# Performance work log

Measured on AMD Instinct MI355X. Metric: run time of the kernel, lower is better.

The kernel has to match this reference:

```python
import jax, jax.numpy as jnp
import numpy as np

N, E = 30000, 180000
IN, H, OUT = 3000, 512, 30


def _segment_softmax(e, dst, n):
    # numerically stable softmax over incoming edges of each destination node
    m = jax.ops.segment_max(e, dst, num_segments=n)
    m = jnp.where(jnp.isfinite(m), m, 0.0)  # nodes with no in-edges
    ex = jnp.exp(e - m[dst])
    den = jax.ops.segment_sum(ex, dst, num_segments=n)
    return ex / den[dst]


def _gat(x, src, dst, Ws, Wd, a_s, a_d, n, alpha=None):
    """edGATConv (heads=1, no self-loops, no bias).
    xs = lin_s(x); attention score from lin_s(x)[src] and lin_d(x)[dst];
    out[i] = sum_{e: dst_e=i} alpha_e * xs[src_e].
    If alpha is given (tie_alpha), reuse it instead of recomputing."""
    xs = x @ Ws.T  # [n, F_out]
    if alpha is None:
        xd = x @ Wd.T
        e = jax.nn.leaky_relu(xs[src] @ a_s + xd[dst] @ a_d, 0.2)  # [E]
        alpha = _segment_softmax(e, dst, n)
    out = jax.ops.segment_sum(alpha[:, None] * xs[src], dst, num_segments=n)
    return out, alpha


def setup_inputs() -> dict:
    key = jax.random.key(0)
    ks = jax.random.split(key, 7)
    features = jax.random.normal(ks[0], (N, IN), dtype=jnp.float32)
    edge_index = jax.random.randint(ks[1], (2, E), 0, N)
    W1s = jax.random.normal(ks[2], (H, IN), dtype=jnp.float32) * 0.02
    W1d = jax.random.normal(ks[3], (H, IN), dtype=jnp.float32) * 0.02
    a1s = jax.random.normal(ks[4], (H,), dtype=jnp.float32) * 0.1
    a1d = jax.random.normal(ks[5], (H,), dtype=jnp.float32) * 0.1
    W2s = jax.random.normal(ks[6], (OUT, H), dtype=jnp.float32) * 0.05
    return {"features": features, "edge_index": edge_index,
            "W1s": W1s, "W1d": W1d, "a1s": a1s, "a1d": a1d, "W2s": W2s}


def reference(features, edge_index, W1s, W1d, a1s, a1d, W2s):
    src, dst = edge_index[0], edge_index[1]
    n = features.shape[0]
    # conv1: attentive GAT layer, stores tie_alpha
    h1, alpha1 = _gat(features, src, dst, W1s, W1d, a1s, a1d, n)
    h1 = jax.nn.elu(h1)
    # conv2: aslinear=True -> plain linear with lin_s
    h2 = h1 @ W2s.T  # [N, OUT]
    # conv3: weights tied to conv2 transposed, alpha tied to conv1
    # W3s = W2s.T so xs3 = h2 @ W3s.T = h2 @ W2s
    h3, _ = _gat(h2, src, dst, W2s.T, None, None, None, n, alpha=alpha1)
    h3 = jax.nn.elu(h3)
    # conv4: aslinear, weight tied to conv1 transposed: h3 @ W4s.T = h3 @ W1s
    h4 = h3 @ W1s  # [N, IN]
    return (h2, h4)
```

## Files before the change

kernel.cpp:

```cpp
#include <hip/hip_runtime.h>

typedef unsigned short u16;
typedef __bf16 bf16_t;
typedef bf16_t bf16x8 __attribute__((ext_vector_type(8)));
typedef float f32x4 __attribute__((ext_vector_type(4)));
typedef u16 u16x8 __attribute__((ext_vector_type(8)));

#define AS1 __attribute__((address_space(1)))
#define AS3 __attribute__((address_space(3)))

__device__ __forceinline__ u16 f2bf(float f) {
    union { float f; unsigned u; } v; v.f = f;
    unsigned r = v.u + 0x7FFFu + ((v.u >> 16) & 1u);
    return (u16)(r >> 16);
}
__device__ __forceinline__ float bf2f(u16 s) {
    union { unsigned u; float f; } v; v.u = ((unsigned)s) << 16;
    return v.f;
}

__device__ __forceinline__ void gload_lds16(const u16* g, u16* l) {
    __builtin_amdgcn_global_load_lds((AS1 const void*)g, (AS3 void*)l, 16, 0, 0);
}

template <bool OUT_BF16, bool GUARD>
__global__ __launch_bounds__(256) void gemm_bt(
    const u16* __restrict__ A, const u16* __restrict__ B, void* __restrict__ Cv,
    int K, int ldc, int Mreal, int Nreal)
{
    __shared__ u16 As[128 * 64];
    __shared__ u16 Bs[128 * 64];
    const int t = threadIdx.x;
    const int w = t >> 6, l = t & 63;

    const int nwg = gridDim.x * gridDim.y;
    const int lin = blockIdx.y * gridDim.x + blockIdx.x;
    const int xcd = lin & 7, loc = lin >> 3;
    const int q = nwg >> 3, r = nwg & 7;
    const int swz = (xcd < r ? xcd * (q + 1) : r * (q + 1) + (xcd - r) * q) + loc;
    const int bx = swz % gridDim.x, by = swz / gridDim.x;

    const int m0 = by * 128, n0 = bx * 128;
    const int wm = (w >> 1) * 64, wn = (w & 1) * 64;

    const int srow = w << 5;
    const int lrow = l >> 3, lc = l & 7;

    f32x4 acc[4][4] = {};

    for (int kt = 0; kt < K; kt += 64) {
#pragma unroll
        for (int i = 0; i < 4; ++i) {
            int row = srow + i * 8 + lrow;
            int gc = ((lc ^ (row & 7)) << 3);
            const u16* ga = A + (size_t)(m0 + row) * K + kt + gc;
            const u16* gb = B + (size_t)(n0 + row) * K + kt + gc;
            u16* la = &As[(srow + i * 8) * 64];
            u16* lb = &Bs[(srow + i * 8) * 64];
            gload_lds16(ga, la);
            gload_lds16(gb, lb);
        }
        asm volatile("s_waitcnt vmcnt(0)");
        __syncthreads();

#pragma unroll
        for (int kk = 0; kk < 2; ++kk) {
            bf16x8 af[4], bfr[4];
            int kc = kk * 4 + (l >> 4);
#pragma unroll
            for (int mi = 0; mi < 4; ++mi) {
                int row = wm + mi * 16 + (l & 15);
                af[mi] = *(const bf16x8*)&As[row * 64 + ((kc ^ (row & 7)) << 3)];
            }
#pragma unroll
            for (int ni = 0; ni < 4; ++ni) {
                int col = wn + ni * 16 + (l & 15);
                bfr[ni] = *(const bf16x8*)&Bs[col * 64 + ((kc ^ (col & 7)) << 3)];
            }
#pragma unroll
            for (int mi = 0; mi < 4; ++mi)
#pragma unroll
                for (int ni = 0; ni < 4; ++ni)
                    acc[mi][ni] = __builtin_amdgcn_mfma_f32_16x16x32_bf16(
                        af[mi], bfr[ni], acc[mi][ni], 0, 0, 0);
        }
        __syncthreads();
    }

#pragma unroll
    for (int mi = 0; mi < 4; ++mi) {
#pragma unroll
        for (int qq = 0; qq < 4; ++qq) {
            int row = m0 + wm + mi * 16 + (l >> 4) * 4 + qq;
            if (GUARD && row >= Mreal) continue;
#pragma unroll
            for (int ni = 0; ni < 4; ++ni) {
                int col = n0 + wn + ni * 16 + (l & 15);
                if (GUARD && col >= Nreal) continue;
                float v = acc[mi][ni][qq];
                if (OUT_BF16) ((u16*)Cv)[(size_t)row * ldc + col] = f2bf(v);
                else          ((float*)Cv)[(size_t)row * ldc + col] = v;
            }
        }
    }
}

__global__ __launch_bounds__(256) void gemm_xw2(
    const float* __restrict__ X, const u16* __restrict__ Bw, u16* __restrict__ C,
    const float* __restrict__ vd, const float* __restrict__ vs,
    float* __restrict__ sd, float* __restrict__ ss)
{
    __shared__ u16 As[128 * 64];
    __shared__ u16 Bs[2][128 * 64];
    const int t = threadIdx.x;
    const int w = t >> 6, l = t & 63;

    const int nwg = gridDim.x * gridDim.y;
    const int lin = blockIdx.y * gridDim.x + blockIdx.x;
    const int xcd = lin & 7, loc = lin >> 3;
    const int q = nwg >> 3, r = nwg & 7;
    const int swz = (xcd < r ? xcd * (q + 1) : r * (q + 1) + (xcd - r) * q) + loc;
    const int bx = swz % gridDim.x, by = swz / gridDim.x;

    const int m0 = by * 128, n0 = bx * 128;
    const int wm = (w >> 1) * 64, wn = (w & 1) * 64;
    const int srow = w << 5;
    const int lrow = l >> 3, lc = l & 7;

    f32x4 acc[4][4] = {};
    float sdp[4] = {}, ssp[4] = {};
    const bool do_s = (bx == 0);

    int rowg[4];
    bool okr[4];
#pragma unroll
    for (int i = 0; i < 4; ++i) {
        rowg[i] = m0 + srow + i * 8 + lrow;
        okr[i] = rowg[i] < 30000;
    }

    float4 pa[4][2];
    auto loadA = [&](int kt) {
        int c = kt + lc * 8;
        bool okc = c < 3000;
#pragma unroll
        for (int i = 0; i < 4; ++i) {
            bool ok = okr[i] && okc;
            const float* p = X + (ok ? ((size_t)rowg[i] * 3000 + c) : 0);
            float4 v0 = *(const float4*)p;
            float4 v1 = *(const float4*)(p + 4);
            if (!ok) { v0 = make_float4(0.f, 0.f, 0.f, 0.f); v1 = v0; }
            pa[i][0] = v0;
            pa[i][1] = v1;
        }
    };
    auto stageB = [&](int kt2, int buf) {
#pragma unroll
        for (int i = 0; i < 4; ++i) {
            int row = srow + i * 8 + lrow;
            int gc = ((lc ^ (row & 7)) << 3);
            gload_lds16(Bw + (size_t)(n0 + row) * 3008 + kt2 + gc,
                        &Bs[buf][(srow + i * 8) * 64]);
        }
    };

    loadA(0);
    stageB(0, 0);
    int cur = 0;

    for (int kt = 0; kt < 3008; kt += 64) {
        if (do_s) {
            int c = kt + lc * 8;
            float4 d0 = *(const float4*)(vd + c);
            float4 d1 = *(const float4*)(vd + c + 4);
            float4 s0 = *(const float4*)(vs + c);
            float4 s1 = *(const float4*)(vs + c + 4);
#pragma unroll
            for (int i = 0; i < 4; ++i) {
                sdp[i] += pa[i][0].x * d0.x + pa[i][0].y * d0.y + pa[i][0].z * d0.z + pa[i][0].w * d0.w
                        + pa[i][1].x * d1.x + pa[i][1].y * d1.y + pa[i][1].z * d1.z + pa[i][1].w * d1.w;
                ssp[i] += pa[i][0].x * s0.x + pa[i][0].y * s0.y + pa[i][0].z * s0.z + pa[i][0].w * s0.w
                        + pa[i][1].x * s1.x + pa[i][1].y * s1.y + pa[i][1].z * s1.z + pa[i][1].w * s1.w;
            }
        }
#pragma unroll
        for (int i = 0; i < 4; ++i) {
            int row = srow + i * 8 + lrow;
            u16x8 o;
            o[0] = f2bf(pa[i][0].x); o[1] = f2bf(pa[i][0].y);
            o[2] = f2bf(pa[i][0].z); o[3] = f2bf(pa[i][0].w);
            o[4] = f2bf(pa[i][1].x); o[5] = f2bf(pa[i][1].y);
            o[6] = f2bf(pa[i][1].z); o[7] = f2bf(pa[i][1].w);
            *(u16x8*)&As[row * 64 + ((lc ^ (row & 7)) << 3)] = o;
        }
        loadA(kt + 64);
        int ktn = (kt + 64 < 3008) ? kt + 64 : 2944;
        stageB(ktn, cur ^ 1);
        asm volatile("s_waitcnt vmcnt(12) lgkmcnt(0)" ::: "memory");
        __builtin_amdgcn_s_barrier();

#pragma unroll
        for (int kk = 0; kk < 2; ++kk) {
            bf16x8 af[4], bfr[4];
            int kc = kk * 4 + (l >> 4);
#pragma unroll
            for (int mi = 0; mi < 4; ++mi) {
                int row = wm + mi * 16 + (l & 15);
                af[mi] = *(const bf16x8*)&As[row * 64 + ((kc ^ (row & 7)) << 3)];
            }
#pragma unroll
            for (int ni = 0; ni < 4; ++ni) {
                int col = wn + ni * 16 + (l & 15);
                bfr[ni] = *(const bf16x8*)&Bs[cur][col * 64 + ((kc ^ (col & 7)) << 3)];
            }
#pragma unroll
            for (int mi = 0; mi < 4; ++mi)
#pragma unroll
                for (int ni = 0; ni < 4; ++ni)
                    acc[mi][ni] = __builtin_amdgcn_mfma_f32_16x16x32_bf16(
                        af[mi], bfr[ni], acc[mi][ni], 0, 0, 0);
        }
        asm volatile("s_barrier" ::: "memory");
        cur ^= 1;
    }

    if (do_s) {
#pragma unroll
        for (int i = 0; i < 4; ++i) {
            float a = sdp[i], b = ssp[i];
            a += __shfl_xor(a, 1); a += __shfl_xor(a, 2); a += __shfl_xor(a, 4);
            b += __shfl_xor(b, 1); b += __shfl_xor(b, 2); b += __shfl_xor(b, 4);
            if (lc == 0 && okr[i]) { sd[rowg[i]] = a; ss[rowg[i]] = b; }
        }
    }

#pragma unroll
    for (int mi = 0; mi < 4; ++mi)
#pragma unroll
        for (int qq = 0; qq < 4; ++qq) {
            int row = m0 + wm + mi * 16 + (l >> 4) * 4 + qq;
#pragma unroll
            for (int ni = 0; ni < 4; ++ni) {
                int col = n0 + wn + ni * 16 + (l & 15);
                C[(size_t)row * 512 + col] = f2bf(acc[mi][qq == 0 ? ni : ni][qq]);
            }
        }
}

__global__ void k_prep(const float* __restrict__ W1d, const float* __restrict__ a1d,
                       const float* __restrict__ W1s, const float* __restrict__ a1s,
                       const float* __restrict__ W2s, const int* __restrict__ dst,
                       float* __restrict__ vd, float* __restrict__ vs,
                       u16* __restrict__ w1sb, u16* __restrict__ w1st,
                       u16* __restrict__ w2sb, unsigned* __restrict__ deg) {
    int b = blockIdx.x, t = threadIdx.x;
    if (b < 12) {
        int i = b * 256 + t;
        if (i >= 3000) return;
        float ad = 0.f, as = 0.f;
        for (int h = 0; h < 512; ++h) {
            ad += W1d[(size_t)h * 3000 + i] * a1d[h];
            as += W1s[(size_t)h * 3000 + i] * a1s[h];
        }
        vd[i] = ad;
        vs[i] = as;
    } else if (b < 1516) {
        int idx = (b - 12) * 256 + t;
        int n = idx / 752, k = (idx % 752) * 4;
        ushort4 o = make_ushort4(0, 0, 0, 0);
        if (k < 3000) {
            float4 v = *(const float4*)(W1s + (size_t)n * 3000 + k);
            o.x = f2bf(v.x); o.y = f2bf(v.y); o.z = f2bf(v.z); o.w = f2bf(v.w);
        }
        *(ushort4*)(w1sb + (size_t)n * 3008 + k) = o;
    } else if (b < 1900) {
        __shared__ float tile[64][65];
        int fb = b - 1516;
        int i0 = (fb % 48) * 64, h0 = (fb / 48) * 64;
        int il = t & 63, hq = t >> 6;
#pragma unroll
        for (int rr = 0; rr < 16; ++rr) {
            int hl = rr * 4 + hq;
            int i = i0 + il;
            tile[hl][il] = (i < 3000) ? W1s[(size_t)(h0 + hl) * 3000 + i] : 0.f;
        }
        __syncthreads();
#pragma unroll
        for (int rr = 0; rr < 16; ++rr) {
            int il2 = rr * 4 + hq;
            w1st[(size_t)(i0 + il2) * 512 + h0 + il] = f2bf(tile[il][il2]);
        }
    } else if (b < 2156) {
        int idx = (b - 1900) * 256 + t;
        int n = idx >> 9, k = idx & 511;
        w2sb[idx] = (n < 30) ? f2bf(W2s[(size_t)n * 512 + k]) : (u16)0;
    } else {
        int j = (b - 2156) * 256 + t;
        if (j < 180000) atomicAdd(&deg[dst[j]], 1u);
    }
}

__global__ void k_scan1(const unsigned* __restrict__ deg, unsigned* __restrict__ bsum, int n) {
    __shared__ unsigned ws[4];
    int i = blockIdx.x * 256 + threadIdx.x;
    unsigned v = (i < n) ? deg[i] : 0u;
#pragma unroll
    for (int s = 32; s; s >>= 1) v += __shfl_xor(v, s);
    if ((threadIdx.x & 63) == 0) ws[threadIdx.x >> 6] = v;
    __syncthreads();
    if (threadIdx.x == 0) bsum[blockIdx.x] = ws[0] + ws[1] + ws[2] + ws[3];
}

__global__ void k_scanB(const unsigned* __restrict__ deg, const unsigned* __restrict__ bsum,
                        unsigned* __restrict__ off, unsigned* __restrict__ cur,
                        int n, int nb) {
    __shared__ unsigned tmp[256];
    __shared__ unsigned bo;
    int b = blockIdx.x, t = threadIdx.x, i = b * 256 + t;
    if (t < 64) {
        unsigned s0 = (t < nb) ? bsum[t] : 0u;
        unsigned s1 = (t + 64 < nb) ? bsum[t + 64] : 0u;
        unsigned v = ((t < b) ? s0 : 0u) + ((t + 64 < b) ? s1 : 0u);
#pragma unroll
        for (int s = 32; s; s >>= 1) v += __shfl_xor(v, s);
        if (t == 0) bo = v;
        if (b == nb - 1) {
            unsigned tv = s0 + s1;
#pragma unroll
            for (int s = 32; s; s >>= 1) tv += __shfl_xor(tv, s);
            if (t == 0) off[n] = tv;
        }
    }
    __syncthreads();
    unsigned v = (i < n) ? deg[i] : 0u;
    tmp[t] = v;
    __syncthreads();
    for (int s = 1; s < 256; s <<= 1) {
        unsigned a = (t >= s) ? tmp[t - s] : 0u;
        __syncthreads();
        tmp[t] += a;
        __syncthreads();
    }
    if (i < n) {
        unsigned o = bo + tmp[t] - v;
        off[i] = o;
        cur[i] = o;
    }
}

__global__ void k_fill(const int* __restrict__ dst, unsigned* __restrict__ cur,
                       unsigned* __restrict__ csr) {
    int j = blockIdx.x * 256 + threadIdx.x;
    if (j >= 180000) return;
    unsigned pos = atomicAdd(&cur[dst[j]], 1u);
    csr[pos] = (unsigned)j;
}

__global__ void k_soft(const int* __restrict__ src, const float* __restrict__ ss,
                       const float* __restrict__ sd, float* __restrict__ alpha,
                       const unsigned* __restrict__ csr, const unsigned* __restrict__ off) {
    int t = threadIdx.x;
    int g = t >> 3, l = t & 7;
    int n = blockIdx.x * 32 + g;
    if (n >= 30000) return;
    unsigned lo = off[n], hi = off[n + 1];
    if (lo == hi) return;
    float sdn = sd[n];
    float m = -1e30f;
    for (unsigned i = lo + l; i < hi; i += 8) {
        float v = ss[src[csr[i]]] + sdn;
        v = v > 0.f ? v : 0.2f * v;
        m = fmaxf(m, v);
    }
    m = fmaxf(m, __shfl_xor(m, 1));
    m = fmaxf(m, __shfl_xor(m, 2));
    m = fmaxf(m, __shfl_xor(m, 4));
    float den = 0.f;
    for (unsigned i = lo + l; i < hi; i += 8) {
        float v = ss[src[csr[i]]] + sdn;
        v = v > 0.f ? v : 0.2f * v;
        den += expf(v - m);
    }
    den += __shfl_xor(den, 1);
    den += __shfl_xor(den, 2);
    den += __shfl_xor(den, 4);
    float inv = 1.f / den;
    for (unsigned i = lo + l; i < hi; i += 8) {
        unsigned j = csr[i];
        float v = ss[src[j]] + sdn;
        v = v > 0.f ? v : 0.2f * v;
        alpha[j] = expf(v - m) * inv;
    }
}

__global__ void k_agg(const u16* __restrict__ xin, const float* __restrict__ alpha,
                      const unsigned* __restrict__ csr, const unsigned* __restrict__ off,
                      const int* __restrict__ src, u16* __restrict__ outb, int nvalid) {
    int w = threadIdx.x >> 6, l = threadIdx.x & 63;
    int n = blockIdx.x * 4 + w;
    float acc[8] = {};
    if (n < nvalid) {
        unsigned lo = off[n], hi = off[n + 1];
        unsigned i = lo;
        for (; i + 2 <= hi; i += 2) {
            unsigned j0 = csr[i], j1 = csr[i + 1];
            float a0 = alpha[j0], a1 = alpha[j1];
            int s0 = src[j0], s1 = src[j1];
            u16x8 r0 = *(const u16x8*)&xin[(size_t)s0 * 512 + l * 8];
            u16x8 r1 = *(const u16x8*)&xin[(size_t)s1 * 512 + l * 8];
#pragma unroll
            for (int k = 0; k < 8; ++k) acc[k] += a0 * bf2f(r0[k]) + a1 * bf2f(r1[k]);
        }
        if (i < hi) {
            unsigned j0 = csr[i];
            float a0 = alpha[j0];
            int s0 = src[j0];
            u16x8 r0 = *(const u16x8*)&xin[(size_t)s0 * 512 + l * 8];
#pragma unroll
            for (int k = 0; k < 8; ++k) acc[k] += a0 * bf2f(r0[k]);
        }
    }
    u16x8 o;
#pragma unroll
    for (int k = 0; k < 8; ++k) {
        float a = acc[k] > 0.f ? acc[k] : expf(acc[k]) - 1.f;
        o[k] = f2bf(a);
    }
    *(u16x8*)&outb[(size_t)n * 512 + l * 8] = o;
}

__global__ void k_aggG(const float* __restrict__ h2, const float* __restrict__ alpha,
                       const unsigned* __restrict__ csr, const unsigned* __restrict__ off,
                       const int* __restrict__ src, float* __restrict__ g) {
    int t = threadIdx.x, grp = t >> 3, l = t & 7;
    int n = blockIdx.x * 32 + grp;
    if (n >= 30000) return;
    unsigned lo = off[n], hi = off[n + 1];
    float acc[4] = {};
    int c0 = l * 4;
    for (unsigned i = lo; i < hi; ++i) {
        unsigned j = csr[i];
        float a = alpha[j];
        const float* row = h2 + (size_t)src[j] * 30;
#pragma unroll
        for (int k = 0; k < 4; ++k) {
            int c = c0 + k;
            if (c < 30) acc[k] += a * row[c];
        }
    }
#pragma unroll
    for (int k = 0; k < 4; ++k) {
        int c = c0 + k;
        if (c < 30) g[(size_t)n * 30 + c] = acc[k];
    }
}

__global__ void k_h3(const float* __restrict__ g, const float* __restrict__ W2s,
                     u16* __restrict__ h3b) {
    int t = threadIdx.x;
    size_t n0 = (size_t)blockIdx.x * 8;
    float w0[30], w1[30];
#pragma unroll
    for (int o = 0; o < 30; ++o) {
        w0[o] = W2s[(size_t)o * 512 + t];
        w1[o] = W2s[(size_t)o * 512 + t + 256];
    }
    for (int rr = 0; rr < 8; ++rr) {
        size_t n = n0 + rr;
        float a0 = 0.f, a1 = 0.f;
        if (n < 30000) {
            const float* gr = g + n * 30;
#pragma unroll
            for (int o = 0; o < 30; ++o) {
                float v = gr[o];
                a0 += v * w0[o];
                a1 += v * w1[o];
            }
            a0 = a0 > 0.f ? a0 : expf(a0) - 1.f;
            a1 = a1 > 0.f ? a1 : expf(a1) - 1.f;
        }
        h3b[n * 512 + t] = f2bf(a0);
        h3b[n * 512 + t + 256] = f2bf(a1);
    }
}

extern "C" void kernel_launch(void* const* d_in, const int* in_sizes, int n_in,
                              void* d_out, int out_size, void* d_ws, size_t ws_size,
                              hipStream_t stream) {
    const float* X   = (const float*)d_in[0];
    const int*   ei  = (const int*)d_in[1];
    const float* W1s = (const float*)d_in[2];
    const float* W1d = (const float*)d_in[3];
    const float* a1s = (const float*)d_in[4];
    const float* a1d = (const float*)d_in[5];
    const float* W2s = (const float*)d_in[6];
    const int* src = ei;
    const int* dst = ei + 180000;

    float* out = (float*)d_out;
    float* h2 = out;
    float* h4 = out + 900000;

    char* ob = (char*)(out + 900000);
    u16* xs1b = (u16*)ob;
    u16* h1b  = (u16*)(ob + 30801920);
    float* g  = (float*)(ob + 30801920 + 30801920);

    char* w = (char*)d_ws;
    auto carve = [&](size_t bytes) { char* p = w; w += (bytes + 255) & ~(size_t)255; return p; };
    u16* w1sb  = (u16*)carve((size_t)512 * 3008 * 2);
    u16* w1st  = (u16*)carve((size_t)3072 * 512 * 2);
    u16* w2sb  = (u16*)carve((size_t)128 * 512 * 2);
    u16* h3b   = (u16*)carve((size_t)30080 * 512 * 2);
    float* vd    = (float*)carve(3008 * 4);
    float* vs    = (float*)carve(3008 * 4);
    float* ss    = (float*)carve(30000 * 4);
    float* sd    = (float*)carve(30000 * 4);
    float* alpha = (float*)carve(180000 * 4);
    unsigned* deg = (unsigned*)carve(30000 * 4);
    unsigned* off = (unsigned*)carve(30004 * 4);
    unsigned* cur = (unsigned*)carve(30000 * 4);
    unsigned* csr = (unsigned*)carve(180000 * 4);
    unsigned* bsum = (unsigned*)carve(128 * 4);

    hipMemsetAsync(deg, 0, 30000 * 4, stream);

    k_prep<<<2860, 256, 0, stream>>>(W1d, a1d, W1s, a1s, W2s, dst,
                                     vd, vs, w1sb, w1st, w2sb, deg);

    gemm_xw2<<<dim3(4, 235), 256, 0, stream>>>(X, w1sb, xs1b, vd, vs, sd, ss);

    k_scan1<<<118, 256, 0, stream>>>(deg, bsum, 30000);
    k_scanB<<<118, 256, 0, stream>>>(deg, bsum, off, cur, 30000, 118);
    k_fill<<<704, 256, 0, stream>>>(dst, cur, csr);
    k_soft<<<938, 256, 0, stream>>>(src, ss, sd, alpha, csr, off);

    k_agg <<<7520, 256, 0, stream>>>(xs1b, alpha, csr, off, src, h1b, 30000);

    gemm_bt<false, true><<<dim3(1, 235), 256, 0, stream>>>(h1b, w2sb, h2, 512, 30, 30000, 30);

    k_aggG<<<938, 256, 0, stream>>>(h2, alpha, csr, off, src, g);
    k_h3 <<<3760, 256, 0, stream>>>(g, W2s, h3b);

    gemm_bt<false, true><<<dim3(24, 235), 256, 0, stream>>>(h3b, w1st, h4, 512, 3000, 30000, 3000);
}
```

Baseline: 645.5 us.

## Convert GEMM kernels to persistent grid-stride tile loops

Both GEMM kernels now loop over virtual tile indices with a grid-stride loop instead of mapping one block to one tile. gemm_xw2 launches 768 blocks for 940 tiles and the h4 GEMM launches 1280 blocks for 5640 tiles. This is meant to cut block launch overhead and even out wave quantization across CUs. The fp32-to-bf16 conversion now uses the native cast, and the padded tail of vd/vs is zeroed. The risk is a tail imbalance where some blocks process one more tile than others.

```diff
diff --git a/kernel.cpp b/kernel.cpp
--- a/kernel.cpp
+++ b/kernel.cpp
@@ -26,80 +26,77 @@
 template <bool OUT_BF16, bool GUARD>
 __global__ __launch_bounds__(256) void gemm_bt(
     const u16* __restrict__ A, const u16* __restrict__ B, void* __restrict__ Cv,
-    int K, int ldc, int Mreal, int Nreal)
+    int K, int ldc, int Mreal, int Nreal, int vgx, int vgy)
 {
     __shared__ u16 As[128 * 64];
     __shared__ u16 Bs[128 * 64];
     const int t = threadIdx.x;
     const int w = t >> 6, l = t & 63;
-
-    const int nwg = gridDim.x * gridDim.y;
-    const int lin = blockIdx.y * gridDim.x + blockIdx.x;
-    const int xcd = lin & 7, loc = lin >> 3;
-    const int q = nwg >> 3, r = nwg & 7;
-    const int swz = (xcd < r ? xcd * (q + 1) : r * (q + 1) + (xcd - r) * q) + loc;
-    const int bx = swz % gridDim.x, by = swz / gridDim.x;
-
-    const int m0 = by * 128, n0 = bx * 128;
     const int wm = (w >> 1) * 64, wn = (w & 1) * 64;
-
     const int srow = w << 5;
     const int lrow = l >> 3, lc = l & 7;
-
-    f32x4 acc[4][4] = {};
-
-    for (int kt = 0; kt < K; kt += 64) {
-#pragma unroll
-        for (int i = 0; i < 4; ++i) {
-            int row = srow + i * 8 + lrow;
-            int gc = ((lc ^ (row & 7)) << 3);
-            const u16* ga = A + (size_t)(m0 + row) * K + kt + gc;
-            const u16* gb = B + (size_t)(n0 + row) * K + kt + gc;
-            u16* la = &As[(srow + i * 8) * 64];
-            u16* lb = &Bs[(srow + i * 8) * 64];
-            gload_lds16(ga, la);
-            gload_lds16(gb, lb);
-        }
-        asm volatile("s_waitcnt vmcnt(0)");
-        __syncthreads();
-
-#pragma unroll
-        for (int kk = 0; kk < 2; ++kk) {
-            bf16x8 af[4], bfr[4];
-            int kc = kk * 4 + (l >> 4);
-#pragma unroll
-            for (int mi = 0; mi < 4; ++mi) {
-                int row = wm + mi * 16 + (l & 15);
-                af[mi] = *(const bf16x8*)&As[row * 64 + ((kc ^ (row & 7)) << 3)];
-            }
-#pragma unroll
-            for (int ni = 0; ni < 4; ++ni) {
-                int col = wn + ni * 16 + (l & 15);
-                bfr[ni] = *(const bf16x8*)&Bs[col * 64 + ((kc ^ (col & 7)) << 3)];
-            }
-#pragma unroll
-            for (int mi = 0; mi < 4; ++mi)
-#pragma unroll
-                for (int ni = 0; ni < 4; ++ni)
-                    acc[mi][ni] = __builtin_amdgcn_mfma_f32_16x16x32_bf16(
-                        af[mi], bfr[ni], acc[mi][ni], 0, 0, 0);
-        }
-        __syncthreads();
-    }
-
-#pragma unroll
-    for (int mi = 0; mi < 4; ++mi) {
-#pragma unroll
-        for (int qq = 0; qq < 4; ++qq) {
-            int row = m0 + wm + mi * 16 + (l >> 4) * 4 + qq;
-            if (GUARD && row >= Mreal) continue;
-#pragma unroll
-            for (int ni = 0; ni < 4; ++ni) {
-                int col = n0 + wn + ni * 16 + (l & 15);
-                if (GUARD && col >= Nreal) continue;
-                float v = acc[mi][ni][qq];
-                if (OUT_BF16) ((u16*)Cv)[(size_t)row * ldc + col] = f2bf(v);
-                else          ((float*)Cv)[(size_t)row * ldc + col] = v;
+    const int nwg = vgx * vgy;
+    const int q = nwg >> 3, r = nwg & 7;
+
+    for (int vb = blockIdx.x; vb < nwg; vb += gridDim.x) {
+        const int xcd = vb & 7, loc = vb >> 3;
+        const int swz = (xcd < r ? xcd * (q + 1) : r * (q + 1) + (xcd - r) * q) + loc;
+        const int bx = swz % vgx, by = swz / vgx;
+        const int m0 = by * 128, n0 = bx * 128;
+
+        f32x4 acc[4][4] = {};
+
+        for (int kt = 0; kt < K; kt += 64) {
+#pragma unroll
+            for (int i = 0; i < 4; ++i) {
+                int row = srow + i * 8 + lrow;
+                int gc = ((lc ^ (row & 7)) << 3);
+                const u16* ga = A + (size_t)(m0 + row) * K + kt + gc;
+                const u16* gb = B + (size_t)(n0 + row) * K + kt + gc;
+                gload_lds16(ga, &As[(srow + i * 8) * 64]);
+                gload_lds16(gb, &Bs[(srow + i * 8) * 64]);
+            }
+            asm volatile("s_waitcnt vmcnt(0)");
+            __syncthreads();
+
+#pragma unroll
+            for (int kk = 0; kk < 2; ++kk) {
+                bf16x8 af[4], bfr[4];
+                int kc = kk * 4 + (l >> 4);
+#pragma unroll
+                for (int mi = 0; mi < 4; ++mi) {
+                    int row = wm + mi * 16 + (l & 15);
+                    af[mi] = *(const bf16x8*)&As[row * 64 + ((kc ^ (row & 7)) << 3)];
+                }
+#pragma unroll
+                for (int ni = 0; ni < 4; ++ni) {
+                    int col = wn + ni * 16 + (l & 15);
+                    bfr[ni] = *(const bf16x8*)&Bs[col * 64 + ((kc ^ (col & 7)) << 3)];
+                }
+#pragma unroll
+                for (int mi = 0; mi < 4; ++mi)
+#pragma unroll
+                    for (int ni = 0; ni < 4; ++ni)
+                        acc[mi][ni] = __builtin_amdgcn_mfma_f32_16x16x32_bf16(
+                            af[mi], bfr[ni], acc[mi][ni], 0, 0, 0);
+            }
+            __syncthreads();
+        }
+
+#pragma unroll
+        for (int mi = 0; mi < 4; ++mi) {
+#pragma unroll
+            for (int qq = 0; qq < 4; ++qq) {
+                int row = m0 + wm + mi * 16 + (l >> 4) * 4 + qq;
+                if (GUARD && row >= Mreal) continue;
+#pragma unroll
+                for (int ni = 0; ni < 4; ++ni) {
+                    int col = n0 + wn + ni * 16 + (l & 15);
+                    if (GUARD && col >= Nreal) continue;
+                    float v = acc[mi][ni][qq];
+                    if (OUT_BF16) ((u16*)Cv)[(size_t)row * ldc + col] = f2bf(v);
+                    else          ((float*)Cv)[(size_t)row * ldc + col] = v;
+                }
             }
         }
     }
@@ -114,137 +111,138 @@
     __shared__ u16 Bs[2][128 * 64];
     const int t = threadIdx.x;
     const int w = t >> 6, l = t & 63;
-
-    const int nwg = gridDim.x * gridDim.y;
-    const int lin = blockIdx.y * gridDim.x + blockIdx.x;
-    const int xcd = lin & 7, loc = lin >> 3;
-    const int q = nwg >> 3, r = nwg & 7;
-    const int swz = (xcd < r ? xcd * (q + 1) : r * (q + 1) + (xcd - r) * q) + loc;
-    const int bx = swz % gridDim.x, by = swz / gridDim.x;
-
-    const int m0 = by * 128, n0 = bx * 128;
     const int wm = (w >> 1) * 64, wn = (w & 1) * 64;
     const int srow = w << 5;
     const int lrow = l >> 3, lc = l & 7;
 
-    f32x4 acc[4][4] = {};
-    float sdp[4] = {}, ssp[4] = {};
-    const bool do_s = (bx == 0);
-
-    int rowg[4];
-    bool okr[4];
-#pragma unroll
-    for (int i = 0; i < 4; ++i) {
-        rowg[i] = m0 + srow + i * 8 + lrow;
-        okr[i] = rowg[i] < 30000;
-    }
-
-    float4 pa[4][2];
-    auto loadA = [&](int kt) {
-        int c = kt + lc * 8;
-        bool okc = c < 3000;
+    const int VGX = 4, NWG = 4 * 235;
+    const int q = NWG >> 3, r = NWG & 7;
+
+    for (int vb = blockIdx.x; vb < NWG; vb += gridDim.x) {
+        const int xcd = vb & 7, loc = vb >> 3;
+        const int swz = (xcd < r ? xcd * (q + 1) : r * (q + 1) + (xcd - r) * q) + loc;
+        const int bx = swz % VGX, by = swz / VGX;
+        const int m0 = by * 128, n0 = bx * 128;
+
+        f32x4 acc[4][4] = {};
+        float sdp[4] = {}, ssp[4] = {};
+        const bool do_s = (bx == 0);
+
+        int rowg[4];
+        bool okr[4];
 #pragma unroll
         for (int i = 0; i < 4; ++i) {
-            bool ok = okr[i] && okc;
-            const float* p = X + (ok ? ((size_t)rowg[i] * 3000 + c) : 0);
-            float4 v0 = *(const float4*)p;
-            float4 v1 = *(const float4*)(p + 4);
-            if (!ok) { v0 = make_float4(0.f, 0.f, 0.f, 0.f); v1 = v0; }
-            pa[i][0] = v0;
-            pa[i][1] = v1;
-        }
-    };
-    auto stageB = [&](int kt2, int buf) {
-#pragma unroll
-        for (int i = 0; i < 4; ++i) {
-            int row = srow + i * 8 + lrow;
-            int gc = ((lc ^ (row & 7)) << 3);
-            gload_lds16(Bw + (size_t)(n0 + row) * 3008 + kt2 + gc,
-                        &Bs[buf][(srow + i * 8) * 64]);
-        }
-    };
-
-    loadA(0);
-    stageB(0, 0);
-    int cur = 0;
-
-    for (int kt = 0; kt < 3008; kt += 64) {
+            rowg[i] = m0 + srow + i * 8 + lrow;
+            okr[i] = rowg[i] < 30000;
+        }
+
+        float4 pa[4][2];
+        auto loadA = [&](int kt) {
+            int c = kt + lc * 8;
+            bool okc = c < 3000;
+#pragma unroll
+            for (int i = 0; i < 4; ++i) {
+                bool ok = okr[i] && okc;
+                const float* p = X + (ok ? ((size_t)rowg[i] * 3000 + c) : 0);
+                float4 v0 = *(const float4*)p;
+                float4 v1 = *(const float4*)(p + 4);
+                if (!ok) { v0 = make_float4(0.f, 0.f, 0.f, 0.f); v1 = v0; }
+                pa[i][0] = v0;
+                pa[i][1] = v1;
+            }
+        };
+        auto stageB = [&](int kt2, int buf) {
+#pragma unroll
+            for (int i = 0; i < 4; ++i) {
+                int row = srow + i * 8 + lrow;
+                int gc = ((lc ^ (row & 7)) << 3);
+                gload_lds16(Bw + (size_t)(n0 + row) * 3008 + kt2 + gc,
+                            &Bs[buf][(srow + i * 8) * 64]);
+            }
+        };
+
+        loadA(0);
+        stageB(0, 0);
+        int cur = 0;
+
+        for (int kt = 0; kt < 3008; kt += 64) {
+            if (do_s) {
+                int c = kt + lc * 8;
+                float4 d0 = *(const float4*)(vd + c);
+                float4 d1 = *(const float4*)(vd + c + 4);
+                float4 s0 = *(const float4*)(vs + c);
+                float4 s1 = *(const float4*)(vs + c + 4);
+#pragma unroll
+                for (int i = 0; i < 4; ++i) {
+                    sdp[i] += pa[i][0].x * d0.x + pa[i][0].y * d0.y + pa[i][0].z * d0.z + pa[i][0].w * d0.w
+                            + pa[i][1].x * d1.x + pa[i][1].y * d1.y + pa[i][1].z * d1.z + pa[i][1].w * d1.w;
+                    ssp[i] += pa[i][0].x * s0.x + pa[i][0].y * s0.y + pa[i][0].z * s0.z + pa[i][0].w * s0.w
+                            + pa[i][1].x * s1.x + pa[i][1].y * s1.y + pa[i][1].z * s1.z + pa[i][1].w * s1.w;
+                }
+            }
+#pragma unroll
+            for (int i = 0; i < 4; ++i) {
+                int row = srow + i * 8 + lrow;
+                bf16x8 o;
+                o[0] = (bf16_t)pa[i][0].x; o[1] = (bf16_t)pa[i][0].y;
+                o[2] = (bf16_t)pa[i][0].z; o[3] = (bf16_t)pa[i][0].w;
+                o[4] = (bf16_t)pa[i][1].x; o[5] = (bf16_t)pa[i][1].y;
+                o[6] = (bf16_t)pa[i][1].z; o[7] = (bf16_t)pa[i][1].w;
+                *(bf16x8*)&As[row * 64 + ((lc ^ (row & 7)) << 3)] = o;
+            }
+            loadA(kt + 64);
+            int ktn = (kt + 64 < 3008) ? kt + 64 : 2944;
+            stageB(ktn, cur ^ 1);
+            asm volatile("s_waitcnt vmcnt(12) lgkmcnt(0)" ::: "memory");
+            __builtin_amdgcn_s_barrier();
+
+#pragma unroll
+            for (int kk = 0; kk < 2; ++kk) {
+                bf16x8 af[4], bfr[4];
+                int kc = kk * 4 + (l >> 4);
+#pragma unroll
+                for (int mi = 0; mi < 4; ++mi) {
+                    int row = wm + mi * 16 + (l & 15);
+                    af[mi] = *(const bf16x8*)&As[row * 64 + ((kc ^ (row & 7)) << 3)];
+                }
+#pragma unroll
+                for (int ni = 0; ni < 4; ++ni) {
+                    int col = wn + ni * 16 + (l & 15);
+                    bfr[ni] = *(const bf16x8*)&Bs[cur][col * 64 + ((kc ^ (col & 7)) << 3)];
+                }
+#pragma unroll
+                for (int mi = 0; mi < 4; ++mi)
+#pragma unroll
+                    for (int ni = 0; ni < 4; ++ni)
+                        acc[mi][ni] = __builtin_amdgcn_mfma_f32_16x16x32_bf16(
+                            af[mi], bfr[ni], acc[mi][ni], 0, 0, 0);
+            }
+            asm volatile("s_barrier" ::: "memory");
+            cur ^= 1;
+        }
+
         if (do_s) {
-            int c = kt + lc * 8;
-            float4 d0 = *(const float4*)(vd + c);
-            float4 d1 = *(const float4*)(vd + c + 4);
-            float4 s0 = *(const float4*)(vs + c);
-            float4 s1 = *(const float4*)(vs + c + 4);
 #pragma unroll
             for (int i = 0; i < 4; ++i) {
-                sdp[i] += pa[i][0].x * d0.x + pa[i][0].y * d0.y + pa[i][0].z * d0.z + pa[i][0].w * d0.w
-                        + pa[i][1].x * d1.x + pa[i][1].y * d1.y + pa[i][1].z * d1.z + pa[i][1].w * d1.w;
-                ssp[i] += pa[i][0].x * s0.x + pa[i][0].y * s0.y + pa[i][0].z * s0.z + pa[i][0].w * s0.w
-                        + pa[i][1].x * s1.x + pa[i][1].y * s1.y + pa[i][1].z * s1.z + pa[i][1].w * s1.w;
-            }
-        }
-#pragma unroll
-        for (int i = 0; i < 4; ++i) {
-            int row = srow + i * 8 + lrow;
-            u16x8 o;
-            o[0] = f2bf(pa[i][0].x); o[1] = f2bf(pa[i][0].y);
-            o[2] = f2bf(pa[i][0].z); o[3] = f2bf(pa[i][0].w);
-            o[4] = f2bf(pa[i][1].x); o[5] = f2bf(pa[i][1].y);
-            o[6] = f2bf(pa[i][1].z); o[7] = f2bf(pa[i][1].w);
-            *(u16x8*)&As[row * 64 + ((lc ^ (row & 7)) << 3)] = o;
-        }
-        loadA(kt + 64);
-        int ktn = (kt + 64 < 3008) ? kt + 64 : 2944;
-        stageB(ktn, cur ^ 1);
-        asm volatile("s_waitcnt vmcnt(12) lgkmcnt(0)" ::: "memory");
-        __builtin_amdgcn_s_barrier();
-
-#pragma unroll
-        for (int kk = 0; kk < 2; ++kk) {
-            bf16x8 af[4], bfr[4];
-            int kc = kk * 4 + (l >> 4);
-#pragma unroll
-            for (int mi = 0; mi < 4; ++mi) {
-                int row = wm + mi * 16 + (l & 15);
-                af[mi] = *(const bf16x8*)&As[row * 64 + ((kc ^ (row & 7)) << 3)];
-            }
-#pragma unroll
-            for (int ni = 0; ni < 4; ++ni) {
-                int col = wn + ni * 16 + (l & 15);
-                bfr[ni] = *(const bf16x8*)&Bs[cur][col * 64 + ((kc ^ (col & 7)) << 3)];
-            }
-#pragma unroll
-            for (int mi = 0; mi < 4; ++mi)
-#pragma unroll
-                for (int ni = 0; ni < 4; ++ni)
-                    acc[mi][ni] = __builtin_amdgcn_mfma_f32_16x16x32_bf16(
-                        af[mi], bfr[ni], acc[mi][ni], 0, 0, 0);
-        }
-        asm volatile("s_barrier" ::: "memory");
-        cur ^= 1;
-    }
-
-    if (do_s) {
-#pragma unroll
-        for (int i = 0; i < 4; ++i) {
-            float a = sdp[i], b = ssp[i];
-            a += __shfl_xor(a, 1); a += __shfl_xor(a, 2); a += __shfl_xor(a, 4);
-            b += __shfl_xor(b, 1); b += __shfl_xor(b, 2); b += __shfl_xor(b, 4);
-            if (lc == 0 && okr[i]) { sd[rowg[i]] = a; ss[rowg[i]] = b; }
-        }
-    }
-
-#pragma unroll
-    for (int mi = 0; mi < 4; ++mi)
-#pragma unroll
-        for (int qq = 0; qq < 4; ++qq) {
-            int row = m0 + wm + mi * 16 + (l >> 4) * 4 + qq;
-#pragma unroll
-            for (int ni = 0; ni < 4; ++ni) {
-                int col = n0 + wn + ni * 16 + (l & 15);
-                C[(size_t)row * 512 + col] = f2bf(acc[mi][qq == 0 ? ni : ni][qq]);
-            }
-        }
+                float a = sdp[i], b = ssp[i];
+                a += __shfl_xor(a, 1); a += __shfl_xor(a, 2); a += __shfl_xor(a, 4);
+                b += __shfl_xor(b, 1); b += __shfl_xor(b, 2); b += __shfl_xor(b, 4);
+                if (lc == 0 && okr[i]) { sd[rowg[i]] = a; ss[rowg[i]] = b; }
+            }
+        }
+
+#pragma unroll
+        for (int mi = 0; mi < 4; ++mi)
+#pragma unroll
+            for (int qq = 0; qq < 4; ++qq) {
+                int row = m0 + wm + mi * 16 + (l >> 4) * 4 + qq;
+#pragma unroll
+                for (int ni = 0; ni < 4; ++ni) {
+                    int col = n0 + wn + ni * 16 + (l & 15);
+                    C[(size_t)row * 512 + col] = f2bf(acc[mi][ni][qq]);
+                }
+            }
+    }
 }
 
 __global__ void k_prep(const float* __restrict__ W1d, const float* __restrict__ a1d,
@@ -256,7 +254,10 @@
     int b = blockIdx.x, t = threadIdx.x;
     if (b < 12) {
         int i = b * 256 + t;
-        if (i >= 3000) return;
+        if (i >= 3000) {
+            if (i < 3008) { vd[i] = 0.f; vs[i] = 0.f; }
+            return;
+        }
         float ad = 0.f, as = 0.f;
         for (int h = 0; h < 512; ++h) {
             ad += W1d[(size_t)h * 3000 + i] * a1d[h];
@@ -528,7 +529,7 @@
     k_prep<<<2860, 256, 0, stream>>>(W1d, a1d, W1s, a1s, W2s, dst,
                                      vd, vs, w1sb, w1st, w2sb, deg);
 
-    gemm_xw2<<<dim3(4, 235), 256, 0, stream>>>(X, w1sb, xs1b, vd, vs, sd, ss);
+    gemm_xw2<<<768, 256, 0, stream>>>(X, w1sb, xs1b, vd, vs, sd, ss);
 
     k_scan1<<<118, 256, 0, stream>>>(deg, bsum, 30000);
     k_scanB<<<118, 256, 0, stream>>>(deg, bsum, off, cur, 30000, 118);
@@ -537,10 +538,10 @@
 
     k_agg <<<7520, 256, 0, stream>>>(xs1b, alpha, csr, off, src, h1b, 30000);
 
-    gemm_bt<false, true><<<dim3(1, 235), 256, 0, stream>>>(h1b, w2sb, h2, 512, 30, 30000, 30);
+    gemm_bt<false, true><<<235, 256, 0, stream>>>(h1b, w2sb, h2, 512, 30, 30000, 30, 1, 235);
 
     k_aggG<<<938, 256, 0, stream>>>(h2, alpha, csr, off, src, g);
     k_h3 <<<3760, 256, 0, stream>>>(g, W2s, h3b);
 
-    gemm_bt<false, true><<<dim3(24, 235), 256, 0, stream>>>(h3b, w1st, h4, 512, 3000, 30000, 3000);
-}
+    gemm_bt<false, true><<<1280, 256, 0, stream>>>(h3b, w1st, h4, 512, 3000, 30000, 3000, 24, 235);
+}
```

New measurement: 640.7 us. Within noise of the previous version (-0.7%).
